# Optimization experiments

Hardware: AMD Instinct MI355X
Metric: run time of the kernel (lower is better)

## Reference

```python
import jax, jax.numpy as jnp
import numpy as np

B, L, D_MODEL = 2, 2048, 1024
D_STATE, D_CONV, EXPAND = 8, 4, 2
D_INNER = EXPAND * D_MODEL          # 2048
DT_RANK = (D_MODEL + 15) // 16      # 64


def setup_inputs() -> dict:
    key = jax.random.key(0)
    ks = jax.random.split(key, 8)
    s = 0.02
    x = jax.random.normal(ks[0], (B, L, D_MODEL), dtype=jnp.float32)
    W_in = jax.random.normal(ks[1], (D_MODEL, 2 * D_INNER), dtype=jnp.float32) * s
    dw_kernel = jax.random.normal(ks[2], (D_CONV, D_INNER), dtype=jnp.float32) * s  # depthwise
    pw_kernel = jax.random.normal(ks[3], (D_INNER, D_INNER), dtype=jnp.float32) * s  # pointwise
    conv_bias = jnp.zeros((D_INNER,), dtype=jnp.float32)
    W_x = jax.random.normal(ks[4], (D_INNER, DT_RANK + 2 * D_STATE), dtype=jnp.float32) * s
    W_dt = jax.random.normal(ks[5], (DT_RANK, D_INNER), dtype=jnp.float32) * s
    b_dt = jnp.zeros((D_INNER,), dtype=jnp.float32)
    # A = repeat(range(1..d_state), d_inner).reshape(d_inner, d_state), stored as log
    A_init = np.repeat(np.arange(1, D_STATE + 1, dtype=np.float32), D_INNER).reshape(D_INNER, D_STATE)
    A_log = jnp.asarray(np.log(A_init))
    D = jnp.ones((D_INNER,), dtype=jnp.float32)
    W_out = jax.random.normal(ks[6], (D_INNER, D_MODEL), dtype=jnp.float32) * s
    return {"x": x, "W_in": W_in, "dw_kernel": dw_kernel, "pw_kernel": pw_kernel,
            "conv_bias": conv_bias, "W_x": W_x, "W_dt": W_dt, "b_dt": b_dt,
            "A_log": A_log, "D": D, "W_out": W_out}


def reference(x, W_in, dw_kernel, pw_kernel, conv_bias, W_x, W_dt, b_dt, A_log, D, W_out):
    d_inner, d_state = A_log.shape
    dt_rank = W_dt.shape[0]
    d_conv = dw_kernel.shape[0]
    bsz = x.shape[0]

    xz = x @ W_in                                   # [B,L,2*di]
    x_in, z = jnp.split(xz, 2, axis=-1)             # each [B,L,di]

    # causal separable conv: depthwise (causal pad) -> pointwise -> swish
    xp = jnp.pad(x_in, ((0, 0), (d_conv - 1, 0), (0, 0)))
    xc = jax.lax.conv_general_dilated(
        xp, dw_kernel[:, None, :], window_strides=(1,), padding='VALID',
        dimension_numbers=('NWC', 'WIO', 'NWC'), feature_group_count=d_inner)
    xc = jax.nn.silu(xc @ pw_kernel + conv_bias)    # [B,L,di]

    x_dbl = xc @ W_x                                # [B,L,dt_rank+2*ds]
    delta = x_dbl[..., :dt_rank]
    Bm = x_dbl[..., dt_rank:dt_rank + d_state]      # [B,L,ds]
    C = x_dbl[..., dt_rank + d_state:]              # [B,L,ds]
    delta = jax.nn.softplus(delta @ W_dt + b_dt)    # [B,L,di]

    A = -jnp.exp(A_log)                             # [di,ds]
    deltaA = jnp.exp(jnp.einsum('bld,dn->bldn', delta, A))       # [B,L,di,ds]
    deltaB_u = jnp.einsum('bld,bln,bld->bldn', delta, Bm, xc)    # [B,L,di,ds]

    def step(h, inp):
        dA_t, dBu_t, C_t = inp
        h = dA_t * h + dBu_t                        # [B,di,ds]
        y_t = jnp.einsum('bn,bdn->bd', C_t, h)      # [B,di]
        return h, y_t

    h0 = jnp.zeros((bsz, d_inner, d_state), dtype=x.dtype)
    elems = (deltaA.transpose(1, 0, 2, 3), deltaB_u.transpose(1, 0, 2, 3), C.transpose(1, 0, 2))
    _, ys = jax.lax.scan(step, h0, elems)           # ys: [L,B,di]
    y = ys.transpose(1, 0, 2)                       # [B,L,di]

    y = y + xc * D
    y = y * jax.nn.silu(z)
    return y @ W_out                                # [B,L,d_model]
```

## Files before the change

kernel.cpp:

```cpp
#include <hip/hip_runtime.h>
#include <math.h>

#define Bb 2
#define Ll 2048
#define DMODEL 1024
#define DINNER 2048
#define DSTATE 8
#define DTRANK 64
#define DCONV 4
#define MM (Bb*Ll)
#define NCH 64
#define CL 32
#define G3_KCH 8
#define G3_KC (DINNER / G3_KCH)

typedef __attribute__((ext_vector_type(8))) short    bf16x8;
typedef __attribute__((ext_vector_type(4))) float    f32x4;

__device__ __forceinline__ float silu_f(float x) {
    return x / (1.0f + __expf(-x));
}
__device__ __forceinline__ float softplus_f(float x) {
    return fmaxf(x, 0.0f) + log1pf(__expf(-fabsf(x)));
}
__device__ __forceinline__ unsigned short f2bf(float f) {
    unsigned int u = __float_as_uint(f);
    u += 0x7fffu + ((u >> 16) & 1u);
    return (unsigned short)(u >> 16);
}
__device__ __forceinline__ float bf2f(unsigned short u) {
    return __uint_as_float(((unsigned int)u) << 16);
}
__device__ __forceinline__ void async_cp16(const unsigned short* g, unsigned short* l) {
    __builtin_amdgcn_global_load_lds(
        (const __attribute__((address_space(1))) void*)g,
        (__attribute__((address_space(3))) void*)l, 16, 0, 0);
}

template <int EPI, typename OT>
__global__ __launch_bounds__(256) void mfma_gemm(
    const unsigned short* __restrict__ A, const unsigned short* __restrict__ Bt,
    OT* __restrict__ C, int M, int N, int K,
    int lda, int ldb, int ldc, const float* __restrict__ bias)
{
    __shared__ unsigned short As[2][128 * 32];
    __shared__ unsigned short Bs[2][128 * 32];

    const int bm = blockIdx.y * 128;
    const int bn = blockIdx.x * 128;
    const int tid  = threadIdx.x;
    const int w    = tid >> 6;
    const int lane = tid & 63;
    const int wm = (w >> 1) * 64;
    const int wn = (w & 1) * 64;
    const int lr = lane & 15;
    const int lq = lane >> 4;

    const int r1 = w * 32 + (lane >> 2);
    const int sp = lane & 3;
    const int slog = sp ^ ((r1 >> 1) & 3);
    const unsigned short* gA1 = A  + (size_t)(bm + r1) * lda + slog * 8;
    const unsigned short* gA2 = gA1 + (size_t)16 * lda;
    const unsigned short* gB1 = Bt + (size_t)(bn + r1) * ldb + slog * 8;
    const unsigned short* gB2 = gB1 + (size_t)16 * ldb;
    const int st1 = w * 1024;
    const int st2 = w * 1024 + 512;

    const int fsw = (lq ^ ((lr >> 1) & 3)) * 8;

    f32x4 acc[4][4];
#pragma unroll
    for (int i = 0; i < 4; ++i)
#pragma unroll
        for (int j = 0; j < 4; ++j) acc[i][j] = (f32x4){0.f, 0.f, 0.f, 0.f};

    async_cp16(gA1, &As[0][st1]);
    async_cp16(gA2, &As[0][st2]);
    async_cp16(gB1, &Bs[0][st1]);
    async_cp16(gB2, &Bs[0][st2]);

    int cur = 0;
    for (int k0 = 0; k0 < K; k0 += 32, cur ^= 1) {
        __syncthreads();
        const int nk = k0 + 32;
        if (nk < K) {
            const int nb = cur ^ 1;
            async_cp16(gA1 + nk, &As[nb][st1]);
            async_cp16(gA2 + nk, &As[nb][st2]);
            async_cp16(gB1 + nk, &Bs[nb][st1]);
            async_cp16(gB2 + nk, &Bs[nb][st2]);
        }

        bf16x8 a[4], b[4];
#pragma unroll
        for (int i = 0; i < 4; ++i)
            a[i] = *(const bf16x8*)&As[cur][(wm + i * 16 + lr) * 32 + fsw];
#pragma unroll
        for (int j = 0; j < 4; ++j)
            b[j] = *(const bf16x8*)&Bs[cur][(wn + j * 16 + lr) * 32 + fsw];
#pragma unroll
        for (int i = 0; i < 4; ++i)
#pragma unroll
            for (int j = 0; j < 4; ++j)
                acc[i][j] = __builtin_amdgcn_mfma_f32_16x16x32_bf16(
                    a[i], b[j], acc[i][j], 0, 0, 0);
    }

#pragma unroll
    for (int i = 0; i < 4; ++i) {
        const int row0 = bm + wm + i * 16 + lq * 4;
#pragma unroll
        for (int j = 0; j < 4; ++j) {
            const int col = bn + wn + j * 16 + lr;
            float bv = (EPI == 1) ? bias[col] : 0.0f;
#pragma unroll
            for (int r = 0; r < 4; ++r) {
                float v = acc[i][j][r];
                if (EPI == 1) v = silu_f(v + bv);
                if (sizeof(OT) == 2)
                    C[(size_t)(row0 + r) * ldc + col] = (OT)f2bf(v);
                else
                    C[(size_t)(row0 + r) * ldc + col] = (OT)v;
            }
        }
    }
}

__global__ __launch_bounds__(256) void gemm_tiled_sp(
    const float* __restrict__ A, const float* __restrict__ B,
    float* __restrict__ C, int M, int N, int K,
    int lda, int ldb, int ldc, const float* __restrict__ bias)
{
    __shared__ float As[16][68];
    __shared__ float Bs[16][68];

    const int bm = blockIdx.y * 64;
    const int bn = blockIdx.x * 64;
    const int tid = threadIdx.x;
    const int tx = tid & 15;
    const int ty = tid >> 4;

    float acc[4][4];
#pragma unroll
    for (int i = 0; i < 4; ++i)
#pragma unroll
        for (int j = 0; j < 4; ++j) acc[i][j] = 0.0f;

    const int ar = tid >> 2;
    const int ac = (tid & 3) << 2;
    const int br = tid >> 4;
    const int bc = (tid & 15) << 2;

    for (int k0 = 0; k0 < K; k0 += 16) {
        float4 av = *(const float4*)&A[(size_t)(bm + ar) * lda + k0 + ac];
        float4 bv = *(const float4*)&B[(size_t)(k0 + br) * ldb + bn + bc];
        As[ac + 0][ar] = av.x;
        As[ac + 1][ar] = av.y;
        As[ac + 2][ar] = av.z;
        As[ac + 3][ar] = av.w;
        *(float4*)&Bs[br][bc] = bv;
        __syncthreads();
#pragma unroll
        for (int k = 0; k < 16; ++k) {
            float4 a4 = *(float4*)&As[k][ty * 4];
            float4 b4 = *(float4*)&Bs[k][tx * 4];
            float am[4] = {a4.x, a4.y, a4.z, a4.w};
            float bn4[4] = {b4.x, b4.y, b4.z, b4.w};
#pragma unroll
            for (int i = 0; i < 4; ++i)
#pragma unroll
                for (int j = 0; j < 4; ++j)
                    acc[i][j] = fmaf(am[i], bn4[j], acc[i][j]);
        }
        __syncthreads();
    }

    const int col = bn + tx * 4;
#pragma unroll
    for (int i = 0; i < 4; ++i) {
        int row = bm + ty * 4 + i;
        float4 v = make_float4(acc[i][0], acc[i][1], acc[i][2], acc[i][3]);
        v.x = softplus_f(v.x + bias[col + 0]);
        v.y = softplus_f(v.y + bias[col + 1]);
        v.z = softplus_f(v.z + bias[col + 2]);
        v.w = softplus_f(v.w + bias[col + 3]);
        *(float4*)&C[(size_t)row * ldc + col] = v;
    }
}

__global__ __launch_bounds__(256) void g3_splitk(
    const unsigned short* __restrict__ xc, const float* __restrict__ Wx,
    float* __restrict__ part)
{
    __shared__ float As[16][68];
    __shared__ float Bs[16][85];
    const int m0 = blockIdx.x * 64;
    const int kb = blockIdx.y * G3_KC;
    const int t = threadIdx.x;
    const int tr = t >> 4;
    const int tc = t & 15;

    const int arow = t >> 2;
    const int ak4  = (t & 3) * 4;
    const int bk   = t >> 4;
    const int bc   = (t & 15) * 5;

    float acc[4][5];
#pragma unroll
    for (int r = 0; r < 4; ++r)
#pragma unroll
        for (int c = 0; c < 5; ++c) acc[r][c] = 0.0f;

    for (int k0 = 0; k0 < G3_KC; k0 += 16) {
        ushort4 av = *(const ushort4*)&xc[(size_t)(m0 + arow) * DINNER + kb + k0 + ak4];
        float bv[5];
#pragma unroll
        for (int q = 0; q < 5; ++q)
            bv[q] = Wx[(size_t)(kb + k0 + bk) * 80 + bc + q];
        __syncthreads();
        As[ak4 + 0][arow] = bf2f(av.x);
        As[ak4 + 1][arow] = bf2f(av.y);
        As[ak4 + 2][arow] = bf2f(av.z);
        As[ak4 + 3][arow] = bf2f(av.w);
#pragma unroll
        for (int q = 0; q < 5; ++q) Bs[bk][bc + q] = bv[q];
        __syncthreads();
#pragma unroll
        for (int k = 0; k < 16; ++k) {
            float a[4], b[5];
#pragma unroll
            for (int r = 0; r < 4; ++r) a[r] = As[k][tr * 4 + r];
#pragma unroll
            for (int c = 0; c < 5; ++c) b[c] = Bs[k][tc * 5 + c];
#pragma unroll
            for (int r = 0; r < 4; ++r)
#pragma unroll
                for (int c = 0; c < 5; ++c)
                    acc[r][c] = fmaf(a[r], b[c], acc[r][c]);
        }
    }
#pragma unroll
    for (int r = 0; r < 4; ++r)
#pragma unroll
        for (int c = 0; c < 5; ++c)
            part[((size_t)blockIdx.y * MM + m0 + tr * 4 + r) * 80 + tc * 5 + c] = acc[r][c];
}

__global__ __launch_bounds__(256) void g3_reduce(
    const float* __restrict__ part, float* __restrict__ xdbl)
{
    int i = (blockIdx.x * 256 + threadIdx.x) * 4;
    if (i >= MM * 80) return;
    float4 s = *(const float4*)&part[i];
#pragma unroll
    for (int c = 1; c < G3_KCH; ++c) {
        float4 p = *(const float4*)&part[(size_t)c * MM * 80 + i];
        s.x += p.x; s.y += p.y; s.z += p.z; s.w += p.w;
    }
    *(float4*)&xdbl[i] = s;
}

__global__ __launch_bounds__(256) void transpose_cast(
    const float* __restrict__ src, unsigned short* __restrict__ dst, int R, int C)
{
    __shared__ float tile[32][33];
    const int c0 = blockIdx.x * 32;
    const int r0 = blockIdx.y * 32;
    const int tx = threadIdx.x;
    const int ty = threadIdx.y;
#pragma unroll
    for (int i = 0; i < 32; i += 8)
        tile[ty + i][tx] = src[(size_t)(r0 + ty + i) * C + c0 + tx];
    __syncthreads();
#pragma unroll
    for (int i = 0; i < 32; i += 8)
        dst[(size_t)(c0 + ty + i) * R + r0 + tx] = f2bf(tile[tx][ty + i]);
}

__global__ __launch_bounds__(256) void cast_bf16(
    const float* __restrict__ src, unsigned short* __restrict__ dst, int n)
{
    int i = (blockIdx.x * 256 + threadIdx.x) * 4;
    if (i >= n) return;
    float4 v = *(const float4*)&src[i];
    ushort4 o;
    o.x = f2bf(v.x); o.y = f2bf(v.y); o.z = f2bf(v.z); o.w = f2bf(v.w);
    *(ushort4*)&dst[i] = o;
}

__global__ __launch_bounds__(256) void dwconv_kernel(
    const float* __restrict__ xz, const float* __restrict__ dwk,
    unsigned short* __restrict__ out)
{
    size_t i = (size_t)blockIdx.x * 256 + threadIdx.x;
    if (i >= (size_t)MM * DINNER) return;
    int d = (int)(i & (DINNER - 1));
    size_t bl = i >> 11;
    int l = (int)(bl & (Ll - 1));
    int b = (int)(bl >> 11);
    float acc = 0.0f;
#pragma unroll
    for (int k = 0; k < DCONV; ++k) {
        int t = l + k - (DCONV - 1);
        if (t >= 0)
            acc = fmaf(xz[((size_t)(b * Ll + t)) * (2 * DINNER) + d],
                       dwk[k * DINNER + d], acc);
    }
    out[i] = f2bf(acc);
}

__global__ __launch_bounds__(256) void scan_pass1(
    const float* __restrict__ delta, const unsigned short* __restrict__ xc,
    const float* __restrict__ xdbl, const float* __restrict__ A_log,
    float* __restrict__ cs_a, float* __restrict__ cs_h)
{
    const int d = blockIdx.x * 256 + threadIdx.x;
    const int c = blockIdx.y;
    const int b = blockIdx.z;
    const int t0 = c * CL;

    __shared__ float sB[CL][8];
    {
        int i = threadIdx.x;
        int t = i >> 3, j = i & 7;
        sB[t][j] = xdbl[((size_t)(b * Ll + t0 + t)) * 80 + DTRANK + j];
    }
    __syncthreads();

    float An[8];
#pragma unroll
    for (int n = 0; n < 8; ++n) An[n] = -__expf(A_log[d * 8 + n]);

    float h[8], ap[8];
#pragma unroll
    for (int n = 0; n < 8; ++n) { h[n] = 0.0f; ap[n] = 1.0f; }

    const float* dptr = delta + ((size_t)(b * Ll + t0)) * DINNER + d;
    const unsigned short* xptr = xc + ((size_t)(b * Ll + t0)) * DINNER + d;

#pragma unroll 4
    for (int t = 0; t < CL; ++t) {
        float dl = dptr[(size_t)t * DINNER];
        float xv = bf2f(xptr[(size_t)t * DINNER]);
        float du = dl * xv;
#pragma unroll
        for (int n = 0; n < 8; ++n) {
            float dA = __expf(dl * An[n]);
            h[n] = fmaf(dA, h[n], du * sB[t][n]);
            ap[n] *= dA;
        }
    }

    size_t base = (((size_t)(b * NCH + c)) * 8) * DINNER + d;
#pragma unroll
    for (int n = 0; n < 8; ++n) {
        cs_a[base + (size_t)n * DINNER] = ap[n];
        cs_h[base + (size_t)n * DINNER] = h[n];
    }
}

__global__ __launch_bounds__(256) void scan_pass2(
    const float* __restrict__ cs_a, const float* cs_h, float* hin)
{
    int idx = blockIdx.x * 256 + threadIdx.x;
    if (idx >= Bb * 8 * DINNER) return;
    int d = idx & (DINNER - 1);
    int n = (idx >> 11) & 7;
    int b = idx >> 14;
    float H = 0.0f;
    for (int c = 0; c < NCH; ++c) {
        size_t o = (((size_t)(b * NCH + c)) * 8 + n) * DINNER + d;
        float a = cs_a[o];
        float hh = cs_h[o];
        hin[o] = H;
        H = fmaf(a, H, hh);
    }
}

__global__ __launch_bounds__(256) void scan_pass3(
    const float* __restrict__ delta, const unsigned short* __restrict__ xc,
    const float* __restrict__ xdbl, const float* __restrict__ A_log,
    const float* __restrict__ hin, const float* __restrict__ xz,
    const float* __restrict__ Dvec, unsigned short* __restrict__ y_bf)
{
    const int d = blockIdx.x * 256 + threadIdx.x;
    const int c = blockIdx.y;
    const int b = blockIdx.z;
    const int t0 = c * CL;

    __shared__ float sB[CL][8];
    __shared__ float sC[CL][8];
    {
        int i = threadIdx.x;
        int t = i >> 4, j = i & 15;
        float v = xdbl[((size_t)(b * Ll + t0 + t)) * 80 + DTRANK + j];
        if (j < 8) sB[t][j] = v; else sC[t][j - 8] = v;
        t = (i + 256) >> 4; j = (i + 256) & 15;
        v = xdbl[((size_t)(b * Ll + t0 + t)) * 80 + DTRANK + j];
        if (j < 8) sB[t][j] = v; else sC[t][j - 8] = v;
    }
    __syncthreads();

    float An[8];
#pragma unroll
    for (int n = 0; n < 8; ++n) An[n] = -__expf(A_log[d * 8 + n]);

    float h[8];
    size_t hbase = (((size_t)(b * NCH + c)) * 8) * DINNER + d;
#pragma unroll
    for (int n = 0; n < 8; ++n) h[n] = hin[hbase + (size_t)n * DINNER];

    const float Dd = Dvec[d];
    const float* dptr = delta + ((size_t)(b * Ll + t0)) * DINNER + d;
    const unsigned short* xptr = xc + ((size_t)(b * Ll + t0)) * DINNER + d;
    const float* zptr = xz + ((size_t)(b * Ll + t0)) * (2 * DINNER) + DINNER + d;
    unsigned short* yptr = y_bf + ((size_t)(b * Ll + t0)) * DINNER + d;

    for (int t = 0; t < CL; ++t) {
        float dl = dptr[(size_t)t * DINNER];
        float xv = bf2f(xptr[(size_t)t * DINNER]);
        float du = dl * xv;
        float yt = 0.0f;
#pragma unroll
        for (int n = 0; n < 8; ++n) {
            float dA = __expf(dl * An[n]);
            h[n] = fmaf(dA, h[n], du * sB[t][n]);
            yt = fmaf(sC[t][n], h[n], yt);
        }
        float zv = zptr[(size_t)t * (2 * DINNER)];
        yptr[(size_t)t * DINNER] = f2bf((yt + xv * Dd) * silu_f(zv));
    }
}

extern "C" void kernel_launch(void* const* d_in, const int* in_sizes, int n_in,
                              void* d_out, int out_size, void* d_ws, size_t ws_size,
                              hipStream_t stream)
{
    const float* x         = (const float*)d_in[0];
    const float* W_in      = (const float*)d_in[1];
    const float* dwk       = (const float*)d_in[2];
    const float* pwk       = (const float*)d_in[3];
    const float* conv_bias = (const float*)d_in[4];
    const float* W_x       = (const float*)d_in[5];
    const float* W_dt      = (const float*)d_in[6];
    const float* b_dt      = (const float*)d_in[7];
    const float* A_log     = (const float*)d_in[8];
    const float* Dv        = (const float*)d_in[9];
    const float* W_out     = (const float*)d_in[10];
    float* out = (float*)d_out;

    char* ws = (char*)d_ws;
    float*          xz     = (float*)(ws);
    unsigned short* x_bf   = (unsigned short*)(ws + (64ull  << 20));
    unsigned short* Wint   = (unsigned short*)(ws + (72ull  << 20));
    float*          g3part = (float*)(ws + (64ull  << 20));
    float*          delta  = (float*)(ws + (64ull  << 20));
    unsigned short* pw_t   = (unsigned short*)(ws + (96ull  << 20));
    float*          cs_a   = (float*)(ws + (96ull  << 20));
    unsigned short* xcp_bf = (unsigned short*)(ws + (104ull << 20));
    float*          cs_h   = (float*)(ws + (104ull << 20));
    unsigned short* Woutt  = (unsigned short*)(ws + (112ull << 20));
    float*          xdbl   = (float*)(ws + (116ull << 20));
    unsigned short* xc_bf  = (unsigned short*)(ws + (120ull << 20));
    unsigned short* y_bf   = (unsigned short*)(ws + (136ull << 20));
    float*          hin    = cs_h;

    dim3 blk(256);

    cast_bf16<<<(MM * DMODEL / 4 + 255) / 256, blk, 0, stream>>>(x, x_bf, MM * DMODEL);
    transpose_cast<<<dim3((2 * DINNER) / 32, DMODEL / 32), dim3(32, 8), 0, stream>>>(
        W_in, Wint, DMODEL, 2 * DINNER);
    transpose_cast<<<dim3(DINNER / 32, DINNER / 32), dim3(32, 8), 0, stream>>>(
        pwk, pw_t, DINNER, DINNER);

    mfma_gemm<0, float><<<dim3((2 * DINNER) / 128, MM / 128), blk, 0, stream>>>(
        x_bf, Wint, xz, MM, 2 * DINNER, DMODEL, DMODEL, DMODEL, 2 * DINNER, nullptr);

    dwconv_kernel<<<(MM * DINNER + 255) / 256, blk, 0, stream>>>(xz, dwk, xcp_bf);

    mfma_gemm<1, unsigned short><<<dim3(DINNER / 128, MM / 128), blk, 0, stream>>>(
        xcp_bf, pw_t, xc_bf, MM, DINNER, DINNER, DINNER, DINNER, DINNER, conv_bias);

    transpose_cast<<<dim3(DMODEL / 32, DINNER / 32), dim3(32, 8), 0, stream>>>(
        W_out, Woutt, DINNER, DMODEL);

    g3_splitk<<<dim3(MM / 64, G3_KCH), blk, 0, stream>>>(xc_bf, W_x, g3part);
    g3_reduce<<<(MM * 80 / 4 + 255) / 256, blk, 0, stream>>>(g3part, xdbl);

    gemm_tiled_sp<<<dim3(DINNER / 64, MM / 64), blk, 0, stream>>>(
        xdbl, W_dt, delta, MM, DINNER, DTRANK, 80, DINNER, DINNER, b_dt);

    scan_pass1<<<dim3(DINNER / 256, NCH, Bb), blk, 0, stream>>>(
        delta, xc_bf, xdbl, A_log, cs_a, cs_h);
    scan_pass2<<<(Bb * 8 * DINNER + 255) / 256, blk, 0, stream>>>(cs_a, cs_h, hin);
    scan_pass3<<<dim3(DINNER / 256, NCH, Bb), blk, 0, stream>>>(
        delta, xc_bf, xdbl, A_log, hin, xz, Dv, y_bf);

    mfma_gemm<0, float><<<dim3(DMODEL / 128, MM / 128), blk, 0, stream>>>(
        y_bf, Woutt, out, MM, DMODEL, DINNER, DINNER, DINNER, DMODEL, nullptr);
}
```

Measured before the change: 419.1 us.

## Emit bf16 split x_in/z from in-proj, 512-thread GEMM, split-K out-proj

The in-projection GEMM now writes x_in and z as separate bf16 arrays instead of one fp32 xz buffer. The depthwise conv and scan_pass3 read these narrower arrays, and the conv is vectorised to four channels per thread. The MFMA GEMM moves to 512-thread blocks with 8 waves, each wave owning a 64x32 sub-tile, for more waves per block. The out-projection becomes a 2-way split-K followed by a reduce kernel to add parallelism. In exchange it adds bf16 rounding of z and x_in, an extra reduce pass, and a reshuffled workspace layout.

Measured after the change: 397.9 us. -5.0%, faster.

```diff
diff --git a/kernel.cpp b/kernel.cpp
--- a/kernel.cpp
+++ b/kernel.cpp
@@ -38,10 +38,11 @@
 }
 
 template <int EPI, typename OT>
-__global__ __launch_bounds__(256) void mfma_gemm(
+__global__ __launch_bounds__(512, 4) void mfma_gemm(
     const unsigned short* __restrict__ A, const unsigned short* __restrict__ Bt,
-    OT* __restrict__ C, int M, int N, int K,
-    int lda, int ldb, int ldc, const float* __restrict__ bias)
+    OT* __restrict__ C, OT* __restrict__ C2, int nsplit, size_t czstride,
+    int M, int N, int K, int lda, int ldb, int ldc,
+    const float* __restrict__ bias)
 {
     __shared__ unsigned short As[2][128 * 32];
     __shared__ unsigned short Bs[2][128 * 32];
@@ -51,33 +52,33 @@
     const int tid  = threadIdx.x;
     const int w    = tid >> 6;
     const int lane = tid & 63;
-    const int wm = (w >> 1) * 64;
-    const int wn = (w & 1) * 64;
+    const int wm = (w >> 2) * 64;
+    const int wn = (w & 3) * 32;
     const int lr = lane & 15;
     const int lq = lane >> 4;
 
-    const int r1 = w * 32 + (lane >> 2);
-    const int sp = lane & 3;
-    const int slog = sp ^ ((r1 >> 1) & 3);
-    const unsigned short* gA1 = A  + (size_t)(bm + r1) * lda + slog * 8;
-    const unsigned short* gA2 = gA1 + (size_t)16 * lda;
-    const unsigned short* gB1 = Bt + (size_t)(bn + r1) * ldb + slog * 8;
-    const unsigned short* gB2 = gB1 + (size_t)16 * ldb;
-    const int st1 = w * 1024;
-    const int st2 = w * 1024 + 512;
+    const size_t kz = (size_t)blockIdx.z * K;
+    A  += kz;
+    Bt += kz;
+    C  += (size_t)blockIdx.z * czstride;
+
+    const int row = tid >> 2;
+    const int sp  = tid & 3;
+    const int slog = sp ^ ((row >> 1) & 3);
+    const unsigned short* gA = A  + (size_t)(bm + row) * lda + slog * 8;
+    const unsigned short* gB = Bt + (size_t)(bn + row) * ldb + slog * 8;
+    const int st = tid * 8;
 
     const int fsw = (lq ^ ((lr >> 1) & 3)) * 8;
 
-    f32x4 acc[4][4];
+    f32x4 acc[4][2];
 #pragma unroll
     for (int i = 0; i < 4; ++i)
 #pragma unroll
-        for (int j = 0; j < 4; ++j) acc[i][j] = (f32x4){0.f, 0.f, 0.f, 0.f};
-
-    async_cp16(gA1, &As[0][st1]);
-    async_cp16(gA2, &As[0][st2]);
-    async_cp16(gB1, &Bs[0][st1]);
-    async_cp16(gB2, &Bs[0][st2]);
+        for (int j = 0; j < 2; ++j) acc[i][j] = (f32x4){0.f, 0.f, 0.f, 0.f};
+
+    async_cp16(gA, &As[0][st]);
+    async_cp16(gB, &Bs[0][st]);
 
     int cur = 0;
     for (int k0 = 0; k0 < K; k0 += 32, cur ^= 1) {
@@ -85,23 +86,21 @@
         const int nk = k0 + 32;
         if (nk < K) {
             const int nb = cur ^ 1;
-            async_cp16(gA1 + nk, &As[nb][st1]);
-            async_cp16(gA2 + nk, &As[nb][st2]);
-            async_cp16(gB1 + nk, &Bs[nb][st1]);
-            async_cp16(gB2 + nk, &Bs[nb][st2]);
-        }
-
-        bf16x8 a[4], b[4];
+            async_cp16(gA + nk, &As[nb][st]);
+            async_cp16(gB + nk, &Bs[nb][st]);
+        }
+
+        bf16x8 a[4], b[2];
 #pragma unroll
         for (int i = 0; i < 4; ++i)
             a[i] = *(const bf16x8*)&As[cur][(wm + i * 16 + lr) * 32 + fsw];
 #pragma unroll
-        for (int j = 0; j < 4; ++j)
+        for (int j = 0; j < 2; ++j)
             b[j] = *(const bf16x8*)&Bs[cur][(wn + j * 16 + lr) * 32 + fsw];
 #pragma unroll
         for (int i = 0; i < 4; ++i)
 #pragma unroll
-            for (int j = 0; j < 4; ++j)
+            for (int j = 0; j < 2; ++j)
                 acc[i][j] = __builtin_amdgcn_mfma_f32_16x16x32_bf16(
                     a[i], b[j], acc[i][j], 0, 0, 0);
     }
@@ -110,20 +109,34 @@
     for (int i = 0; i < 4; ++i) {
         const int row0 = bm + wm + i * 16 + lq * 4;
 #pragma unroll
-        for (int j = 0; j < 4; ++j) {
+        for (int j = 0; j < 2; ++j) {
             const int col = bn + wn + j * 16 + lr;
+            OT* Cb; int colb;
+            if (col < nsplit) { Cb = C; colb = col; }
+            else              { Cb = C2; colb = col - nsplit; }
             float bv = (EPI == 1) ? bias[col] : 0.0f;
 #pragma unroll
             for (int r = 0; r < 4; ++r) {
                 float v = acc[i][j][r];
                 if (EPI == 1) v = silu_f(v + bv);
                 if (sizeof(OT) == 2)
-                    C[(size_t)(row0 + r) * ldc + col] = (OT)f2bf(v);
+                    Cb[(size_t)(row0 + r) * ldc + colb] = (OT)f2bf(v);
                 else
-                    C[(size_t)(row0 + r) * ldc + col] = (OT)v;
+                    Cb[(size_t)(row0 + r) * ldc + colb] = (OT)v;
             }
         }
     }
+}
+
+__global__ __launch_bounds__(256) void g5_reduce(
+    const float* __restrict__ part, float* __restrict__ out, int n)
+{
+    int i = (blockIdx.x * 256 + threadIdx.x) * 4;
+    if (i >= n) return;
+    float4 a = *(const float4*)&part[i];
+    float4 b = *(const float4*)&part[(size_t)n + i];
+    a.x += b.x; a.y += b.y; a.z += b.z; a.w += b.w;
+    *(float4*)&out[i] = a;
 }
 
 __global__ __launch_bounds__(256) void gemm_tiled_sp(
@@ -289,24 +302,31 @@
 }
 
 __global__ __launch_bounds__(256) void dwconv_kernel(
-    const float* __restrict__ xz, const float* __restrict__ dwk,
+    const unsigned short* __restrict__ x_in, const float* __restrict__ dwk,
     unsigned short* __restrict__ out)
 {
-    size_t i = (size_t)blockIdx.x * 256 + threadIdx.x;
-    if (i >= (size_t)MM * DINNER) return;
-    int d = (int)(i & (DINNER - 1));
-    size_t bl = i >> 11;
-    int l = (int)(bl & (Ll - 1));
-    int b = (int)(bl >> 11);
-    float acc = 0.0f;
+    int i4 = blockIdx.x * 256 + threadIdx.x;
+    if (i4 >= MM * DINNER / 4) return;
+    int d = (i4 * 4) & (DINNER - 1);
+    int bl = (i4 * 4) >> 11;
+    int l = bl & (Ll - 1);
+    int b = bl >> 11;
+    float a0 = 0.f, a1 = 0.f, a2 = 0.f, a3 = 0.f;
 #pragma unroll
     for (int k = 0; k < DCONV; ++k) {
         int t = l + k - (DCONV - 1);
-        if (t >= 0)
-            acc = fmaf(xz[((size_t)(b * Ll + t)) * (2 * DINNER) + d],
-                       dwk[k * DINNER + d], acc);
-    }
-    out[i] = f2bf(acc);
+        if (t >= 0) {
+            ushort4 xv = *(const ushort4*)&x_in[(size_t)(b * Ll + t) * DINNER + d];
+            float4 wv = *(const float4*)&dwk[k * DINNER + d];
+            a0 = fmaf(bf2f(xv.x), wv.x, a0);
+            a1 = fmaf(bf2f(xv.y), wv.y, a1);
+            a2 = fmaf(bf2f(xv.z), wv.z, a2);
+            a3 = fmaf(bf2f(xv.w), wv.w, a3);
+        }
+    }
+    ushort4 o;
+    o.x = f2bf(a0); o.y = f2bf(a1); o.z = f2bf(a2); o.w = f2bf(a3);
+    *(ushort4*)&out[i4 * 4] = o;
 }
 
 __global__ __launch_bounds__(256) void scan_pass1(
@@ -380,7 +400,7 @@
 __global__ __launch_bounds__(256) void scan_pass3(
     const float* __restrict__ delta, const unsigned short* __restrict__ xc,
     const float* __restrict__ xdbl, const float* __restrict__ A_log,
-    const float* __restrict__ hin, const float* __restrict__ xz,
+    const float* __restrict__ hin, const unsigned short* __restrict__ z,
     const float* __restrict__ Dvec, unsigned short* __restrict__ y_bf)
 {
     const int d = blockIdx.x * 256 + threadIdx.x;
@@ -413,7 +433,7 @@
     const float Dd = Dvec[d];
     const float* dptr = delta + ((size_t)(b * Ll + t0)) * DINNER + d;
     const unsigned short* xptr = xc + ((size_t)(b * Ll + t0)) * DINNER + d;
-    const float* zptr = xz + ((size_t)(b * Ll + t0)) * (2 * DINNER) + DINNER + d;
+    const unsigned short* zptr = z + ((size_t)(b * Ll + t0)) * DINNER + d;
     unsigned short* yptr = y_bf + ((size_t)(b * Ll + t0)) * DINNER + d;
 
     for (int t = 0; t < CL; ++t) {
@@ -427,7 +447,7 @@
             h[n] = fmaf(dA, h[n], du * sB[t][n]);
             yt = fmaf(sC[t][n], h[n], yt);
         }
-        float zv = zptr[(size_t)t * (2 * DINNER)];
+        float zv = bf2f(zptr[(size_t)t * DINNER]);
         yptr[(size_t)t * DINNER] = f2bf((yt + xv * Dd) * silu_f(zv));
     }
 }
@@ -450,39 +470,43 @@
     float* out = (float*)d_out;
 
     char* ws = (char*)d_ws;
-    float*          xz     = (float*)(ws);
-    unsigned short* x_bf   = (unsigned short*)(ws + (64ull  << 20));
-    unsigned short* Wint   = (unsigned short*)(ws + (72ull  << 20));
-    float*          g3part = (float*)(ws + (64ull  << 20));
-    float*          delta  = (float*)(ws + (64ull  << 20));
-    unsigned short* pw_t   = (unsigned short*)(ws + (96ull  << 20));
-    float*          cs_a   = (float*)(ws + (96ull  << 20));
-    unsigned short* xcp_bf = (unsigned short*)(ws + (104ull << 20));
-    float*          cs_h   = (float*)(ws + (104ull << 20));
-    unsigned short* Woutt  = (unsigned short*)(ws + (112ull << 20));
-    float*          xdbl   = (float*)(ws + (116ull << 20));
-    unsigned short* xc_bf  = (unsigned short*)(ws + (120ull << 20));
-    unsigned short* y_bf   = (unsigned short*)(ws + (136ull << 20));
-    float*          hin    = cs_h;
+    unsigned short* x_in_bf = (unsigned short*)(ws);
+    unsigned short* z_bf    = (unsigned short*)(ws + (16ull << 20));
+    float*          delta   = (float*)(ws + (32ull << 20));
+    float*          g5part  = (float*)(ws + (32ull << 20));
+    unsigned short* x_bf    = (unsigned short*)(ws + (64ull << 20));
+    unsigned short* y_bf    = (unsigned short*)(ws + (64ull << 20));
+    unsigned short* Wint    = (unsigned short*)(ws + (72ull << 20));
+    unsigned short* pw_t    = (unsigned short*)(ws + (80ull << 20));
+    unsigned short* xcp_bf  = (unsigned short*)(ws + (88ull << 20));
+    unsigned short* xc_bf   = (unsigned short*)(ws + (104ull << 20));
+    unsigned short* Woutt   = (unsigned short*)(ws + (120ull << 20));
+    float*          xdbl    = (float*)(ws + (124ull << 20));
+    float*          g3part  = (float*)(ws + (126ull << 20));
+    float*          cs_a    = (float*)(ws + (136ull << 20));
+    float*          cs_h    = (float*)(ws + (144ull << 20));
+    float*          hin     = cs_h;
 
     dim3 blk(256);
+    dim3 blk512(512);
 
     cast_bf16<<<(MM * DMODEL / 4 + 255) / 256, blk, 0, stream>>>(x, x_bf, MM * DMODEL);
     transpose_cast<<<dim3((2 * DINNER) / 32, DMODEL / 32), dim3(32, 8), 0, stream>>>(
         W_in, Wint, DMODEL, 2 * DINNER);
     transpose_cast<<<dim3(DINNER / 32, DINNER / 32), dim3(32, 8), 0, stream>>>(
         pwk, pw_t, DINNER, DINNER);
-
-    mfma_gemm<0, float><<<dim3((2 * DINNER) / 128, MM / 128), blk, 0, stream>>>(
-        x_bf, Wint, xz, MM, 2 * DINNER, DMODEL, DMODEL, DMODEL, 2 * DINNER, nullptr);
-
-    dwconv_kernel<<<(MM * DINNER + 255) / 256, blk, 0, stream>>>(xz, dwk, xcp_bf);
-
-    mfma_gemm<1, unsigned short><<<dim3(DINNER / 128, MM / 128), blk, 0, stream>>>(
-        xcp_bf, pw_t, xc_bf, MM, DINNER, DINNER, DINNER, DINNER, DINNER, conv_bias);
-
     transpose_cast<<<dim3(DMODEL / 32, DINNER / 32), dim3(32, 8), 0, stream>>>(
         W_out, Woutt, DINNER, DMODEL);
+
+    mfma_gemm<0, unsigned short><<<dim3((2 * DINNER) / 128, MM / 128, 1), blk512, 0, stream>>>(
+        x_bf, Wint, x_in_bf, z_bf, DINNER, 0,
+        MM, 2 * DINNER, DMODEL, DMODEL, DMODEL, DINNER, nullptr);
+
+    dwconv_kernel<<<MM * DINNER / 4 / 256, blk, 0, stream>>>(x_in_bf, dwk, xcp_bf);
+
+    mfma_gemm<1, unsigned short><<<dim3(DINNER / 128, MM / 128, 1), blk512, 0, stream>>>(
+        xcp_bf, pw_t, xc_bf, xc_bf, DINNER + 1, 0,
+        MM, DINNER, DINNER, DINNER, DINNER, DINNER, conv_bias);
 
     g3_splitk<<<dim3(MM / 64, G3_KCH), blk, 0, stream>>>(xc_bf, W_x, g3part);
     g3_reduce<<<(MM * 80 / 4 + 255) / 256, blk, 0, stream>>>(g3part, xdbl);
@@ -494,8 +518,11 @@
         delta, xc_bf, xdbl, A_log, cs_a, cs_h);
     scan_pass2<<<(Bb * 8 * DINNER + 255) / 256, blk, 0, stream>>>(cs_a, cs_h, hin);
     scan_pass3<<<dim3(DINNER / 256, NCH, Bb), blk, 0, stream>>>(
-        delta, xc_bf, xdbl, A_log, hin, xz, Dv, y_bf);
-
-    mfma_gemm<0, float><<<dim3(DMODEL / 128, MM / 128), blk, 0, stream>>>(
-        y_bf, Woutt, out, MM, DMODEL, DINNER, DINNER, DINNER, DMODEL, nullptr);
-}
+        delta, xc_bf, xdbl, A_log, hin, z_bf, Dv, y_bf);
+
+    mfma_gemm<0, float><<<dim3(DMODEL / 128, MM / 128, 2), blk512, 0, stream>>>(
+        y_bf, Woutt, g5part, g5part, DMODEL + 1, (size_t)MM * DMODEL,
+        MM, DMODEL, DINNER / 2, DINNER, DINNER, DMODEL, nullptr);
+    g5_reduce<<<(MM * DMODEL / 4 + 255) / 256, blk, 0, stream>>>(
+        g5part, out, MM * DMODEL);
+}
```
